# Kernel optimization log

Measured on AMD Instinct MI355X. Metric: run time of the kernel, lower is better.

## Reference

```python
import jax, jax.numpy as jnp
import numpy as np

NORM_EPS = 1e-05

def _quant_input(x):
    # per-token dynamic int8 fake-quant: s = 127 / max(|x|, 1e-5)
    s = 127.0 / jnp.clip(jnp.max(jnp.abs(x), axis=-1, keepdims=True), 1e-05, None)
    return jnp.clip(jnp.round(x * s), -128.0, 127.0) / s

def _rmsnorm(x, w, eps):
    return x * jax.lax.rsqrt(jnp.mean(x * x, axis=-1, keepdims=True) + eps) * w

def setup_inputs() -> dict:
    key = jax.random.key(0)
    k0, k1, k2 = jax.random.split(key, 3)
    dim, hidden = 2048, 5632
    x = jax.random.normal(k0, (4, 2048, dim), dtype=jnp.float32)
    w13 = jax.random.normal(k1, (2 * hidden, dim), dtype=jnp.float32) * 0.02
    w2 = jax.random.normal(k2, (dim, hidden), dtype=jnp.float32) * 0.02
    norm_w = jnp.ones((hidden,), dtype=jnp.float32)
    return {"x": x, "w13": w13, "w2": w2, "norm_w": norm_w}

def reference(x, w13, w2, norm_w):
    # BitLinear w13: quantize input, then linear
    xq = _quant_input(x)
    x13 = jnp.einsum('bsd,fd->bsf', xq, w13)  # [B,S,2H]
    x1, x3 = jnp.split(x13, 2, axis=-1)
    gated = jnp.square(jax.nn.relu(x1)) * x3  # squared-ReLU gating
    inner = _rmsnorm(gated, norm_w, NORM_EPS)
    # BitLinear w2
    iq = _quant_input(inner)
    out = jnp.einsum('bsh,dh->bsd', iq, w2)
    return out
```

## Files before the change

### kernel.cpp

```cpp
#include <hip/hip_runtime.h>

typedef unsigned short u16;
typedef __attribute__((ext_vector_type(8))) short short8;
typedef __attribute__((ext_vector_type(4))) float f32x4;
typedef __attribute__((ext_vector_type(4))) u16 ushort4v;
typedef __attribute__((ext_vector_type(8))) u16 ushort8v;

#define DIM 2048
#define HID 5632
#define F2  11264
#define TTOT 8192

#define GLD(g, l) __builtin_amdgcn_global_load_lds(                       \
    (const __attribute__((address_space(1))) void*)(g),                   \
    (__attribute__((address_space(3))) void*)(l), 16, 0, 0)

__device__ __forceinline__ u16 f2bf(float f) {
  unsigned int u = __builtin_bit_cast(unsigned int, f);
  u += 0x7FFFu + ((u >> 16) & 1u);
  return (u16)(u >> 16);
}

__global__ __launch_bounds__(256) void conv_w13(const float* __restrict__ w,
                                                u16* __restrict__ o) {
  int idx = blockIdx.x * 256 + threadIdx.x;
  int rnew = idx >> 9;
  int dc = (idx & 511) << 2;
  int b = rnew >> 5, ii = rnew & 31;
  int orig = (ii < 16) ? (b * 16 + ii) : (HID + b * 16 + (ii - 16));
  float4 v = *reinterpret_cast<const float4*>(w + (size_t)orig * DIM + dc);
  ushort4v q = {f2bf(v.x), f2bf(v.y), f2bf(v.z), f2bf(v.w)};
  *reinterpret_cast<ushort4v*>(o + (size_t)rnew * DIM + dc) = q;
}

__global__ __launch_bounds__(256) void conv_w2(const float* __restrict__ w,
                                               u16* __restrict__ o) {
  size_t e = ((size_t)blockIdx.x * 256 + threadIdx.x) * 4;
  float4 v = *reinterpret_cast<const float4*>(w + e);
  ushort4v q = {f2bf(v.x), f2bf(v.y), f2bf(v.z), f2bf(v.w)};
  *reinterpret_cast<ushort4v*>(o + e) = q;
}

__global__ __launch_bounds__(256) void quant_x(const float* __restrict__ x,
                                               u16* __restrict__ q,
                                               float* __restrict__ scale) {
  const int t = blockIdx.x;
  const float* xr = x + (size_t)t * DIM;
  const int tid = threadIdx.x;
  float4 a = *reinterpret_cast<const float4*>(xr + tid * 8);
  float4 b = *reinterpret_cast<const float4*>(xr + tid * 8 + 4);
  float v[8] = {a.x, a.y, a.z, a.w, b.x, b.y, b.z, b.w};
  float m = 0.f;
#pragma unroll
  for (int i = 0; i < 8; ++i) m = fmaxf(m, fabsf(v[i]));
#pragma unroll
  for (int off = 32; off; off >>= 1) m = fmaxf(m, __shfl_xor(m, off));
  __shared__ float red[4];
  if ((tid & 63) == 0) red[tid >> 6] = m;
  __syncthreads();
  m = fmaxf(fmaxf(red[0], red[1]), fmaxf(red[2], red[3]));
  m = fmaxf(m, 1e-5f);
  float s = 127.0f / m;
  if (tid == 0) scale[t] = m / 127.0f;
  ushort8v o;
#pragma unroll
  for (int i = 0; i < 8; ++i) {
    float r = fminf(fmaxf(rintf(v[i] * s), -128.f), 127.f);
    o[i] = f2bf(r);
  }
  *reinterpret_cast<ushort8v*>(q + (size_t)t * DIM + tid * 8) = o;
}

__global__ __launch_bounds__(256) void gate_nq(const float* __restrict__ G,
                                               const float* __restrict__ nw,
                                               u16* __restrict__ q2,
                                               float* __restrict__ s2) {
  const int t = blockIdx.x;
  const float* gr = G + (size_t)t * HID;
  const int tid = threadIdx.x;
  float4 vv[6];
  float ss = 0.f, mx = 0.f;
#pragma unroll
  for (int k = 0; k < 6; ++k) {
    int i = tid + k * 256;
    if (i < 1408) {
      float4 v = *reinterpret_cast<const float4*>(gr + i * 4);
      float4 w4 = *reinterpret_cast<const float4*>(nw + i * 4);
      vv[k] = v;
      ss += v.x * v.x + v.y * v.y + v.z * v.z + v.w * v.w;
      mx = fmaxf(mx, fmaxf(fmaxf(fabsf(v.x * w4.x), fabsf(v.y * w4.y)),
                           fmaxf(fabsf(v.z * w4.z), fabsf(v.w * w4.w))));
    }
  }
#pragma unroll
  for (int off = 32; off; off >>= 1) {
    ss += __shfl_xor(ss, off);
    mx = fmaxf(mx, __shfl_xor(mx, off));
  }
  __shared__ float rs[4], rm[4];
  if ((tid & 63) == 0) { rs[tid >> 6] = ss; rm[tid >> 6] = mx; }
  __syncthreads();
  ss = rs[0] + rs[1] + rs[2] + rs[3];
  mx = fmaxf(fmaxf(rm[0], rm[1]), fmaxf(rm[2], rm[3]));
  float rinv = 1.0f / sqrtf(ss * (1.0f / 5632.0f) + 1e-5f);
  float mi = fmaxf(mx * rinv, 1e-5f);
  float s = 127.0f / mi;
  if (tid == 0) s2[t] = mi / 127.0f;
  float fs = rinv * s;
#pragma unroll
  for (int k = 0; k < 6; ++k) {
    int i = tid + k * 256;
    if (i < 1408) {
      float4 v = vv[k];
      float4 w4 = *reinterpret_cast<const float4*>(nw + i * 4);
      ushort4v o;
      o.x = f2bf(fminf(fmaxf(rintf(v.x * w4.x * fs), -128.f), 127.f));
      o.y = f2bf(fminf(fmaxf(rintf(v.y * w4.y * fs), -128.f), 127.f));
      o.z = f2bf(fminf(fmaxf(rintf(v.z * w4.z * fs), -128.f), 127.f));
      o.w = f2bf(fminf(fmaxf(rintf(v.w * w4.w * fs), -128.f), 127.f));
      *reinterpret_cast<ushort4v*>(q2 + (size_t)t * HID + i * 4) = o;
    }
  }
}

template <int GATE, int N, int K, int Ntiles>
__global__ __launch_bounds__(512, 2) void gemm8(
    const u16* __restrict__ A, const u16* __restrict__ B,
    const float* __restrict__ rowscale, float* __restrict__ C, int panel) {
  __shared__ __attribute__((aligned(16))) u16 lds[2][2][2][256 * 32];
  constexpr int NT = K >> 6;
  const int nwg = gridDim.x;
  const int orig = blockIdx.x;
  const int qq = nwg >> 3, rr = nwg & 7, xcd = orig & 7, sidx = orig >> 3;
  const int wg = (xcd < rr ? xcd * (qq + 1) : rr * (qq + 1) + (xcd - rr) * qq) + sidx;
  const int stripe = panel * Ntiles;
  const int mt = (wg / stripe) * panel + (wg % panel);
  const int nt = (wg % stripe) / panel;

  const int tid = threadIdx.x;
  const int wid = tid >> 6, lane = tid & 63;
  const int wm = wid >> 2, wn = wid & 3;
  const int c16 = lane & 15, q4 = lane >> 4;
  const int rA_base = wm * 128 + c16;
  const int rB_base = wn * 64 + c16;
  const int caf = (q4 ^ ((lane >> 1) & 3)) << 3;

  const int sr = tid >> 2;
  const int scol = ((tid & 3) ^ ((tid >> 3) & 3)) << 3;
  const u16* Ar = A + ((size_t)mt * 256 + sr) * K + scol;
  const u16* Br = B + ((size_t)nt * 256 + sr) * K + scol;
  constexpr size_t rstep = (size_t)128 * K;

  f32x4 acc[8][4];
#pragma unroll
  for (int m = 0; m < 8; ++m)
#pragma unroll
    for (int n = 0; n < 4; ++n) acc[m][n] = f32x4{0.f, 0.f, 0.f, 0.f};

#define STAGE(MAT, KK, T, BUF)                                                \
  {                                                                           \
    const u16* g = ((MAT) ? Br : Ar) + (T) * 64 + (KK) * 32;                  \
    u16* l = &lds[BUF][MAT][KK][wid << 9];                                    \
    GLD(g, l);                                                                \
    GLD(g + rstep, l + 4096);                                                 \
  }
#define LDA(DB, KK, MH, AF)                                                   \
  _Pragma("unroll") for (int m = 0; m < 4; ++m)                               \
      AF[m] = *reinterpret_cast<const short8*>(                               \
          &lds[DB][0][KK][(rA_base + ((MH) * 4 + m) * 16) * 32 + caf]);
#define LDB(DB, KK, BF)                                                       \
  _Pragma("unroll") for (int n = 0; n < 4; ++n)                               \
      BF[n] = *reinterpret_cast<const short8*>(                               \
          &lds[DB][1][KK][(rB_base + n * 16) * 32 + caf]);
#define MFMA32(AF0, AF1, BF)                                                  \
  __builtin_amdgcn_s_setprio(1);                                              \
  _Pragma("unroll") for (int m = 0; m < 4; ++m)                               \
      _Pragma("unroll") for (int n = 0; n < 4; ++n)                           \
          acc[m][n] = __builtin_amdgcn_mfma_f32_16x16x32_bf16(                \
              AF0[m], BF[n], acc[m][n], 0, 0, 0);                             \
  _Pragma("unroll") for (int m = 0; m < 4; ++m)                               \
      _Pragma("unroll") for (int n = 0; n < 4; ++n)                           \
          acc[4 + m][n] = __builtin_amdgcn_mfma_f32_16x16x32_bf16(            \
              AF1[m], BF[n], acc[4 + m][n], 0, 0, 0);                         \
  __builtin_amdgcn_s_setprio(0);                                              \
  __builtin_amdgcn_sched_barrier(0);
#define BARR asm volatile("s_barrier" ::: "memory")
#define VMC(NN) asm volatile("s_waitcnt vmcnt(" #NN ")" ::: "memory")
#define NOPW do {} while (0)

#define KT2(DB, U, STGA, STGB, WB)                                            \
  {                                                                           \
    short8 bfr[4], af0[4], af1[4];                                            \
                                                            \
    if (STGA) {                                                               \
      STAGE(0, 1, (U) + 1, (DB) ^ 1)                                          \
      STAGE(1, 1, (U) + 1, (DB) ^ 1)                                          \
    }                                                                         \
    LDB(DB, 0, bfr)                                                           \
    LDA(DB, 0, 0, af0)                                                        \
    LDA(DB, 0, 1, af1)                                                        \
    MFMA32(af0, af1, bfr)                                                     \
    BARR;                                                                     \
                                                            \
    if (STGB) {                                                               \
      STAGE(0, 0, (U) + 2, DB)                                                \
      STAGE(1, 0, (U) + 2, DB)                                                \
    }                                                                         \
    LDB(DB, 1, bfr)                                                           \
    LDA(DB, 1, 0, af0)                                                        \
    LDA(DB, 1, 1, af1)                                                        \
    MFMA32(af0, af1, bfr)                                                     \
    WB;                                                                       \
    BARR;                                                                     \
  }

  STAGE(1, 0, 0, 0) STAGE(0, 0, 0, 0) STAGE(1, 1, 0, 0) STAGE(0, 1, 0, 0)
  STAGE(1, 0, 1, 1) STAGE(0, 0, 1, 1)
  VMC(4);
  BARR;

#pragma unroll 1
  for (int u = 0; u < NT - 2; u += 2) {
    KT2(0, u, 1, 1, VMC(4))
    KT2(1, u + 1, 1, 1, VMC(4))
  }
  KT2(0, NT - 2, 1, 0, VMC(0))
  KT2(1, NT - 1, 0, 0, NOPW)

  const int mbase0 = mt * 256 + wm * 128;
  if constexpr (GATE == 0) {
#pragma unroll
    for (int m = 0; m < 8; ++m) {
#pragma unroll
      for (int j = 0; j < 4; ++j) {
        const int row = mbase0 + m * 16 + q4 * 4 + j;
        const float sc = rowscale[row];
        float* crow = C + (size_t)row * N + nt * 256 + wn * 64 + c16;
#pragma unroll
        for (int n = 0; n < 4; ++n) crow[n * 16] = acc[m][n][j] * sc;
      }
    }
  } else {
    constexpr int H = N >> 1;
    const int gbase = (nt * 256 + wn * 64) >> 1;
#pragma unroll
    for (int m = 0; m < 8; ++m) {
#pragma unroll
      for (int j = 0; j < 4; ++j) {
        const int row = mbase0 + m * 16 + q4 * 4 + j;
        const float sc = rowscale[row];
        const float s3 = sc * sc * sc;
        float* grow = C + (size_t)row * H + gbase + c16;
#pragma unroll
        for (int p = 0; p < 2; ++p) {
          float a1 = acc[m][2 * p][j];
          float a3 = acc[m][2 * p + 1][j];
          float rl = fmaxf(a1, 0.f);
          grow[p * 16] = rl * rl * a3 * s3;
        }
      }
    }
  }
}

extern "C" void kernel_launch(void* const* d_in, const int* in_sizes, int n_in,
                              void* d_out, int out_size, void* d_ws, size_t ws_size,
                              hipStream_t stream) {
  const float* x = (const float*)d_in[0];
  const float* w13 = (const float*)d_in[1];
  const float* w2 = (const float*)d_in[2];
  const float* nw = (const float*)d_in[3];
  float* out = (float*)d_out;

  char* p = (char*)d_ws;
  u16* w13p = (u16*)p; p += (size_t)F2 * DIM * 2;
  u16* w2b = (u16*)p;  p += (size_t)DIM * HID * 2;
  u16* q2f = (u16*)p;  p += (size_t)TTOT * HID * 2;
  float* s2f = (float*)p; p += (size_t)TTOT * 4;
  const size_t fixed = (size_t)F2 * DIM * 2 + (size_t)DIM * HID * 2 +
                       (size_t)TTOT * HID * 2 + (size_t)TTOT * 4;
  const size_t perTok = (size_t)DIM * 2 + (size_t)HID * 4 + 8;
  int Tc = TTOT;
  while (Tc > 256 && fixed + (size_t)Tc * perTok > ws_size) Tc >>= 1;
  u16* q1 = (u16*)p;        p += (size_t)Tc * DIM * 2;
  float* gated = (float*)p; p += (size_t)Tc * HID * 4;
  float* s1 = (float*)p;

  conv_w13<<<F2 * DIM / 4 / 256, 256, 0, stream>>>(w13, w13p);
  conv_w2<<<DIM * HID / 4 / 256, 256, 0, stream>>>(w2, w2b);

  const int mtiles1 = Tc / 256;
  const int panel1 = mtiles1 < 8 ? mtiles1 : 8;
  for (int t0 = 0; t0 < TTOT; t0 += Tc) {
    quant_x<<<Tc, 256, 0, stream>>>(x + (size_t)t0 * DIM, q1, s1);
    gemm8<1, F2, DIM, F2 / 256><<<(Tc / 256) * (F2 / 256), 512, 0, stream>>>(
        q1, w13p, s1, gated, panel1);
    gate_nq<<<Tc, 256, 0, stream>>>(gated, nw, q2f + (size_t)t0 * HID, s2f + t0);
  }
  gemm8<0, DIM, HID, DIM / 256><<<(TTOT / 256) * (DIM / 256), 512, 0, stream>>>(
      q2f, w2b, s2f, out, 8);
}
```

Before: 581.0 us.

## Split each K-tile into four MFMA quadrants with interleaved LDS reads and staging

Restructures the GEMM main-loop body so each 64-wide K tile is computed as four quadrant MFMA groups (A-half × B-half), each preceded by barrier-separated LDS fragment reads and one global-to-LDS staging load. This spreads staging and LDS traffic across more phases, in the style of HipKittens 8-wave ping-pong, so memory work overlaps MFMA execution better. The cost is more barriers and explicit lgkmcnt waits per tile, plus more live fragment registers, which could stall the pipeline or reduce occupancy.

```diff
diff --git a/kernel.cpp b/kernel.cpp
--- a/kernel.cpp
+++ b/kernel.cpp
@@ -168,50 +168,56 @@
   _Pragma("unroll") for (int m = 0; m < 4; ++m)                               \
       AF[m] = *reinterpret_cast<const short8*>(                               \
           &lds[DB][0][KK][(rA_base + ((MH) * 4 + m) * 16) * 32 + caf]);
-#define LDB(DB, KK, BF)                                                       \
-  _Pragma("unroll") for (int n = 0; n < 4; ++n)                               \
+#define LDB2(DB, KK, NH, BF)                                                  \
+  _Pragma("unroll") for (int n = 0; n < 2; ++n)                               \
       BF[n] = *reinterpret_cast<const short8*>(                               \
-          &lds[DB][1][KK][(rB_base + n * 16) * 32 + caf]);
-#define MFMA32(AF0, AF1, BF)                                                  \
+          &lds[DB][1][KK][(rB_base + ((NH) * 2 + n) * 16) * 32 + caf]);
+#define MFMAQ(AK0, AK1, BK0, BK1, MOFS, NOFS)                                 \
   __builtin_amdgcn_s_setprio(1);                                              \
   _Pragma("unroll") for (int m = 0; m < 4; ++m)                               \
-      _Pragma("unroll") for (int n = 0; n < 4; ++n)                           \
-          acc[m][n] = __builtin_amdgcn_mfma_f32_16x16x32_bf16(                \
-              AF0[m], BF[n], acc[m][n], 0, 0, 0);                             \
+      _Pragma("unroll") for (int n = 0; n < 2; ++n)                           \
+          acc[(MOFS) + m][(NOFS) + n] = __builtin_amdgcn_mfma_f32_16x16x32_bf16( \
+              AK0[m], BK0[n], acc[(MOFS) + m][(NOFS) + n], 0, 0, 0);          \
   _Pragma("unroll") for (int m = 0; m < 4; ++m)                               \
-      _Pragma("unroll") for (int n = 0; n < 4; ++n)                           \
-          acc[4 + m][n] = __builtin_amdgcn_mfma_f32_16x16x32_bf16(            \
-              AF1[m], BF[n], acc[4 + m][n], 0, 0, 0);                         \
+      _Pragma("unroll") for (int n = 0; n < 2; ++n)                           \
+          acc[(MOFS) + m][(NOFS) + n] = __builtin_amdgcn_mfma_f32_16x16x32_bf16( \
+              AK1[m], BK1[n], acc[(MOFS) + m][(NOFS) + n], 0, 0, 0);          \
   __builtin_amdgcn_s_setprio(0);                                              \
   __builtin_amdgcn_sched_barrier(0);
 #define BARR asm volatile("s_barrier" ::: "memory")
 #define VMC(NN) asm volatile("s_waitcnt vmcnt(" #NN ")" ::: "memory")
+#define LGKM0 do { asm volatile("s_waitcnt lgkmcnt(0)" ::: "memory");         \
+                   __builtin_amdgcn_sched_barrier(0); } while (0)
 #define NOPW do {} while (0)
 
-#define KT2(DB, U, STGA, STGB, WB)                                            \
+#define KT4(DB, U, STG12, STG34, WB)                                          \
   {                                                                           \
-    short8 bfr[4], af0[4], af1[4];                                            \
-                                                            \
-    if (STGA) {                                                               \
-      STAGE(0, 1, (U) + 1, (DB) ^ 1)                                          \
-      STAGE(1, 1, (U) + 1, (DB) ^ 1)                                          \
-    }                                                                         \
-    LDB(DB, 0, bfr)                                                           \
-    LDA(DB, 0, 0, af0)                                                        \
-    LDA(DB, 0, 1, af1)                                                        \
-    MFMA32(af0, af1, bfr)                                                     \
+    short8 a0k0[4], a0k1[4], a1k0[4], a1k1[4];                                \
+    short8 b0k0[2], b0k1[2], b1k0[2], b1k1[2];                                \
+                                                             \
+    LDA(DB, 0, 0, a0k0) LDA(DB, 1, 0, a0k1)                                   \
+    LDB2(DB, 0, 0, b0k0) LDB2(DB, 1, 0, b0k1)                                 \
+    if (STG12) { STAGE(1, 1, (U) + 1, (DB) ^ 1) }                             \
+    BARR; LGKM0;                                                              \
+    MFMAQ(a0k0, a0k1, b0k0, b0k1, 0, 0)                                       \
     BARR;                                                                     \
-                                                            \
-    if (STGB) {                                                               \
-      STAGE(0, 0, (U) + 2, DB)                                                \
-      STAGE(1, 0, (U) + 2, DB)                                                \
-    }                                                                         \
-    LDB(DB, 1, bfr)                                                           \
-    LDA(DB, 1, 0, af0)                                                        \
-    LDA(DB, 1, 1, af1)                                                        \
-    MFMA32(af0, af1, bfr)                                                     \
-    WB;                                                                       \
+                                             \
+    LDB2(DB, 0, 1, b1k0) LDB2(DB, 1, 1, b1k1)                                 \
+    if (STG12) { STAGE(0, 1, (U) + 1, (DB) ^ 1) }                             \
+    BARR; LGKM0;                                                              \
+    MFMAQ(a0k0, a0k1, b1k0, b1k1, 0, 2)                                       \
     BARR;                                                                     \
+                                             \
+    LDA(DB, 0, 1, a1k0) LDA(DB, 1, 1, a1k1)                                   \
+    if (STG34) { STAGE(1, 0, (U) + 2, DB) }                                   \
+    BARR; LGKM0;                                                              \
+    MFMAQ(a1k0, a1k1, b0k0, b0k1, 4, 0)                                       \
+    BARR;                                                                     \
+                                    \
+    if (STG34) { STAGE(0, 0, (U) + 2, DB) }                                   \
+    BARR;                                                                     \
+    MFMAQ(a1k0, a1k1, b1k0, b1k1, 4, 2)                                       \
+    WB; BARR;                                                                 \
   }
 
   STAGE(1, 0, 0, 0) STAGE(0, 0, 0, 0) STAGE(1, 1, 0, 0) STAGE(0, 1, 0, 0)
@@ -221,11 +227,11 @@
 
 #pragma unroll 1
   for (int u = 0; u < NT - 2; u += 2) {
-    KT2(0, u, 1, 1, VMC(4))
-    KT2(1, u + 1, 1, 1, VMC(4))
-  }
-  KT2(0, NT - 2, 1, 0, VMC(0))
-  KT2(1, NT - 1, 0, 0, NOPW)
+    KT4(0, u, 1, 1, VMC(4))
+    KT4(1, u + 1, 1, 1, VMC(4))
+  }
+  KT4(0, NT - 2, 1, 0, VMC(0))
+  KT4(1, NT - 1, 0, 0, NOPW)
 
   const int mbase0 = mt * 256 + wm * 128;
   if constexpr (GATE == 0) {
```

Result: no change. 571.1 us (-1.7%).

## Load GEMM B operand directly from global into registers, bypassing LDS

Applied to the files above, without the earlier changes.

The GEMM kernel now stages only the A tile through LDS with global_load_lds. Each wave reads its B fragments straight from global memory into registers. This halves LDS use and the LDS read traffic for B, and drops the explicit vmcnt waits from the pipeline. In exchange, B rows are fetched separately by the two wave rows that share them, and load latency is exposed. The compiler's inserted waits on the B loads may also end up waiting on the in-flight A staging loads, which would serialize the prefetch pipeline.

```diff
diff --git a/kernel.cpp b/kernel.cpp
--- a/kernel.cpp
+++ b/kernel.cpp
@@ -127,7 +127,7 @@
 __global__ __launch_bounds__(512, 2) void gemm8(
     const u16* __restrict__ A, const u16* __restrict__ B,
     const float* __restrict__ rowscale, float* __restrict__ C, int panel) {
-  __shared__ __attribute__((aligned(16))) u16 lds[2][2][2][256 * 32];
+  __shared__ __attribute__((aligned(16))) u16 lds[2][2][256 * 32];
   constexpr int NT = K >> 6;
   const int nwg = gridDim.x;
   const int orig = blockIdx.x;
@@ -142,36 +142,36 @@
   const int wm = wid >> 2, wn = wid & 3;
   const int c16 = lane & 15, q4 = lane >> 4;
   const int rA_base = wm * 128 + c16;
-  const int rB_base = wn * 64 + c16;
   const int caf = (q4 ^ ((lane >> 1) & 3)) << 3;
 
   const int sr = tid >> 2;
   const int scol = ((tid & 3) ^ ((tid >> 3) & 3)) << 3;
   const u16* Ar = A + ((size_t)mt * 256 + sr) * K + scol;
-  const u16* Br = B + ((size_t)nt * 256 + sr) * K + scol;
   constexpr size_t rstep = (size_t)128 * K;
 
+  const u16* Bg = B + ((size_t)(nt * 256 + wn * 64 + c16)) * K + q4 * 8;
+
   f32x4 acc[8][4];
 #pragma unroll
   for (int m = 0; m < 8; ++m)
 #pragma unroll
     for (int n = 0; n < 4; ++n) acc[m][n] = f32x4{0.f, 0.f, 0.f, 0.f};
 
-#define STAGE(MAT, KK, T, BUF)                                                \
+#define STAGE(KK, T, BUF)                                                     \
   {                                                                           \
-    const u16* g = ((MAT) ? Br : Ar) + (T) * 64 + (KK) * 32;                  \
-    u16* l = &lds[BUF][MAT][KK][wid << 9];                                    \
+    const u16* g = Ar + (T) * 64 + (KK) * 32;                                 \
+    u16* l = &lds[BUF][KK][wid << 9];                                         \
     GLD(g, l);                                                                \
     GLD(g + rstep, l + 4096);                                                 \
   }
 #define LDA(DB, KK, MH, AF)                                                   \
   _Pragma("unroll") for (int m = 0; m < 4; ++m)                               \
       AF[m] = *reinterpret_cast<const short8*>(                               \
-          &lds[DB][0][KK][(rA_base + ((MH) * 4 + m) * 16) * 32 + caf]);
-#define LDB(DB, KK, BF)                                                       \
+          &lds[DB][KK][(rA_base + ((MH) * 4 + m) * 16) * 32 + caf]);
+#define LDBG(U, KK, BF)                                                       \
   _Pragma("unroll") for (int n = 0; n < 4; ++n)                               \
       BF[n] = *reinterpret_cast<const short8*>(                               \
-          &lds[DB][1][KK][(rB_base + n * 16) * 32 + caf]);
+          Bg + (size_t)n * 16 * K + (U) * 64 + (KK) * 32);
 #define MFMA32(AF0, AF1, BF)                                                  \
   __builtin_amdgcn_s_setprio(1);                                              \
   _Pragma("unroll") for (int m = 0; m < 4; ++m)                               \
@@ -186,46 +186,38 @@
   __builtin_amdgcn_sched_barrier(0);
 #define BARR asm volatile("s_barrier" ::: "memory")
 #define VMC(NN) asm volatile("s_waitcnt vmcnt(" #NN ")" ::: "memory")
-#define NOPW do {} while (0)
-
-#define KT2(DB, U, STGA, STGB, WB)                                            \
+
+#define KT2(DB, U, STGA, STGB)                                                \
   {                                                                           \
-    short8 bfr[4], af0[4], af1[4];                                            \
+    short8 af0[4], af1[4], bk0[4], bk1[4];                                    \
                                                             \
-    if (STGA) {                                                               \
-      STAGE(0, 1, (U) + 1, (DB) ^ 1)                                          \
-      STAGE(1, 1, (U) + 1, (DB) ^ 1)                                          \
-    }                                                                         \
-    LDB(DB, 0, bfr)                                                           \
+    if (STGA) { STAGE(1, (U) + 1, (DB) ^ 1) }                                 \
+    LDBG((U), 0, bk0)                                                         \
+    LDBG((U), 1, bk1)                                                         \
     LDA(DB, 0, 0, af0)                                                        \
     LDA(DB, 0, 1, af1)                                                        \
-    MFMA32(af0, af1, bfr)                                                     \
+    MFMA32(af0, af1, bk0)                                                     \
     BARR;                                                                     \
                                                             \
-    if (STGB) {                                                               \
-      STAGE(0, 0, (U) + 2, DB)                                                \
-      STAGE(1, 0, (U) + 2, DB)                                                \
-    }                                                                         \
-    LDB(DB, 1, bfr)                                                           \
+    if (STGB) { STAGE(0, (U) + 2, DB) }                                       \
     LDA(DB, 1, 0, af0)                                                        \
     LDA(DB, 1, 1, af1)                                                        \
-    MFMA32(af0, af1, bfr)                                                     \
-    WB;                                                                       \
+    MFMA32(af0, af1, bk1)                                                     \
     BARR;                                                                     \
   }
 
-  STAGE(1, 0, 0, 0) STAGE(0, 0, 0, 0) STAGE(1, 1, 0, 0) STAGE(0, 1, 0, 0)
-  STAGE(1, 0, 1, 1) STAGE(0, 0, 1, 1)
-  VMC(4);
+  STAGE(0, 0, 0) STAGE(1, 0, 0)
+  STAGE(0, 1, 1)
+  VMC(2);
   BARR;
 
 #pragma unroll 1
   for (int u = 0; u < NT - 2; u += 2) {
-    KT2(0, u, 1, 1, VMC(4))
-    KT2(1, u + 1, 1, 1, VMC(4))
-  }
-  KT2(0, NT - 2, 1, 0, VMC(0))
-  KT2(1, NT - 1, 0, 0, NOPW)
+    KT2(0, u, 1, 1)
+    KT2(1, u + 1, 1, 1)
+  }
+  KT2(0, NT - 2, 1, 0)
+  KT2(1, NT - 1, 0, 0)
 
   const int mbase0 = mt * 256 + wm * 128;
   if constexpr (GATE == 0) {
```

After: 993.1 us. 70.9% more time.
